# Kernel tuning notes

Hardware: AMD Instinct MI355X
Metric: run time of the kernel (lower is better)

The kernel has to match this reference:

```python
import jax, jax.numpy as jnp
import numpy as np

IN_DIM = 2
HID = 256
OUT_DIM = 1
B = 131072


def setup_inputs() -> dict:
    key = jax.random.key(0)
    ks = jax.random.split(key, 9)
    def glorot(k, shape):
        fan_in = shape[0]
        return jax.random.normal(k, shape, dtype=jnp.float32) / jnp.sqrt(jnp.float32(fan_in))
    return {
        "x": jax.random.normal(ks[0], (B, IN_DIM), dtype=jnp.float32),
        "W1": glorot(ks[1], (IN_DIM, HID)), "b1": jnp.zeros((HID,), jnp.float32),
        "W2": glorot(ks[2], (HID, HID)),    "b2": jnp.zeros((HID,), jnp.float32),
        "W3": glorot(ks[3], (HID, HID)),    "b3": jnp.zeros((HID,), jnp.float32),
        "W4": glorot(ks[4], (HID, OUT_DIM)),"b4": jnp.zeros((OUT_DIM,), jnp.float32),
    }


def reference(x, W1, b1, W2, b2, W3, b3, W4, b4):
    # Inner PINN model: tanh MLP, per-sample fn (IN_DIM,) -> (OUT_DIM,)
    def f(xi):
        h = jnp.tanh(xi @ W1 + b1)
        h = jnp.tanh(h @ W2 + b2)
        h = jnp.tanh(h @ W3 + b3)
        return h @ W4 + b4

    # Original layer computes full batch_jacobian then slices column 0.
    # Mathematically this is the directional derivative along e0, computed
    # here directly with forward-mode JVPs (same values, no wasted columns).
    e0 = jnp.zeros((IN_DIM,), x.dtype).at[0].set(1.0)

    def du_dx0(xi):  # (OUT_DIM,) : d u / d x[0]
        return jax.jvp(f, (xi,), (e0,))[1]

    def per_point(xi):
        u = f(xi)                                   # (OUT_DIM,)
        du, d2u = jax.jvp(du_dx0, (xi,), (e0,))     # du/dx0, d2u/dx0^2
        return u, du, d2u

    return jax.vmap(per_point)(x)  # each (B, OUT_DIM)
```

## Files before the change

kernel.cpp:

```cpp
#include <hip/hip_runtime.h>


#define HID 256
#define TM  32
#define LDK 264

typedef _Float16 half8 __attribute__((ext_vector_type(8)));
typedef _Float16 half4 __attribute__((ext_vector_type(4)));
typedef float    f32x4 __attribute__((ext_vector_type(4)));

__device__ __forceinline__ float fast_tanh(float z) {
    const float e = __expf(2.0f * z);
#if __has_builtin(__builtin_amdgcn_rcpf)
    const float r = __builtin_amdgcn_rcpf(e + 1.0f);
#else
    const float r = 1.0f / (e + 1.0f);
#endif
    return fmaf(-2.0f, r, 1.0f);
}

__global__ __launch_bounds__(256) void prep_w(const float* __restrict__ W2,
                                              const float* __restrict__ W3,
                                              _Float16* __restrict__ wsf) {
    const int t = blockIdx.x * 256 + threadIdx.x;
    const float* __restrict__ W = (t >> 13) ? W3 : W2;
    _Float16* hi = wsf + (size_t)(t >> 13) * 65536;
    const int r    = t & 8191;
    const int nt   = r >> 9;
    const int kc   = (r >> 6) & 7;
    const int lane = r & 63;
    const int row  = kc * 32 + ((lane >> 4) << 3);
    const int col  = nt * 16 + (lane & 15);
    half8 vh;
    #pragma unroll
    for (int j = 0; j < 8; ++j)
        vh[j] = (_Float16)W[(size_t)(row + j) * HID + col];
    *(half8*)&hi[(size_t)r * 8] = vh;
}

__global__ __launch_bounds__(512, 4) void pinn_mfma(
    const float* __restrict__ x,
    const float* __restrict__ W1, const float* __restrict__ b1,
    const float* __restrict__ b2, const float* __restrict__ b3,
    const float* __restrict__ W4, const float* __restrict__ b4,
    const _Float16* __restrict__ wsf,
    float* __restrict__ out, int B)
{
    __shared__ __align__(16) _Float16 Ahi[3][TM][LDK];
    __shared__ float psumW[8][3][TM];

    const int tid  = threadIdx.x;
    const int s0   = blockIdx.x * TM;
    const int lane = tid & 63;
    const int wave = tid >> 6;

    {
        const int m  = tid >> 4;
        const int k0 = (tid & 15) * 16;
        const float x0 = x[(s0 + m) * 2 + 0];
        const float x1 = x[(s0 + m) * 2 + 1];
        half8 vh[3][2];
        #pragma unroll
        for (int hfi = 0; hfi < 2; ++hfi) {
            #pragma unroll
            for (int j = 0; j < 8; ++j) {
                const int n = k0 + hfi * 8 + j;
                const float w0 = W1[n];
                const float w1 = W1[HID + n];
                const float z  = fmaf(x0, w0, fmaf(x1, w1, b1[n]));
                const float a  = fast_tanh(z);
                const float sN = 1.0f - a * a;
                const float ad  = sN * w0;
                const float add = -2.0f * a * ad * w0;
                vh[0][hfi][j] = (_Float16)a;
                vh[1][hfi][j] = (_Float16)ad;
                vh[2][hfi][j] = (_Float16)add;
            }
        }
        #pragma unroll
        for (int s = 0; s < 3; ++s) {
            *(half8*)&Ahi[s][m][k0]     = vh[s][0];
            *(half8*)&Ahi[s][m][k0 + 8] = vh[s][1];
        }
    }
    __syncthreads();

    const int ml = lane & 15;
    const int kq = (lane >> 4) * 8;
    const int u4 = (lane >> 4) * 4;

    #pragma unroll 1
    for (int layer = 0; layer < 2; ++layer) {
        const _Float16* __restrict__ Wh = wsf + (size_t)layer * 65536;

        f32x4 acc[3][2][2];
        #pragma unroll
        for (int s = 0; s < 3; ++s)
            #pragma unroll
            for (int nt = 0; nt < 2; ++nt)
                #pragma unroll
                for (int mt = 0; mt < 2; ++mt)
                    acc[s][nt][mt] = (f32x4){0.f, 0.f, 0.f, 0.f};

        #pragma unroll 1
        for (int kc = 0; kc < 8; ++kc) {
            half8 ah[3][2];
            #pragma unroll
            for (int s = 0; s < 3; ++s)
                #pragma unroll
                for (int mt = 0; mt < 2; ++mt)
                    ah[s][mt] = *(const half8*)&Ahi[s][mt * 16 + ml][kc * 32 + kq];
            #pragma unroll
            for (int nt = 0; nt < 2; ++nt) {
                const int strip = wave * 2 + nt;
                const size_t fi = ((size_t)((strip * 8 + kc) * 64 + lane)) * 8;
                const half8 wh = *(const half8*)&Wh[fi];
                #pragma unroll
                for (int mt = 0; mt < 2; ++mt) {
                    acc[0][nt][mt] = __builtin_amdgcn_mfma_f32_16x16x32_f16(wh, ah[0][mt], acc[0][nt][mt], 0, 0, 0);
                    acc[1][nt][mt] = __builtin_amdgcn_mfma_f32_16x16x32_f16(wh, ah[1][mt], acc[1][nt][mt], 0, 0, 0);
                    acc[2][nt][mt] = __builtin_amdgcn_mfma_f32_16x16x32_f16(wh, ah[2][mt], acc[2][nt][mt], 0, 0, 0);
                }
            }
        }

        __syncthreads();

        if (layer == 0) {
            #pragma unroll
            for (int nt = 0; nt < 2; ++nt) {
                const int ub = wave * 32 + nt * 16 + u4;
                const f32x4 bb = *(const f32x4*)&b2[ub];
                #pragma unroll
                for (int mt = 0; mt < 2; ++mt) {
                    half4 hv[3];
                    #pragma unroll
                    for (int r = 0; r < 4; ++r) {
                        const float z   = acc[0][nt][mt][r] + bb[r];
                        const float a   = fast_tanh(z);
                        const float sN  = 1.0f - a * a;
                        const float zd  = acc[1][nt][mt][r];
                        const float zdd = acc[2][nt][mt][r];
                        const float ad  = sN * zd;
                        const float add = fmaf(sN, zdd, -2.0f * a * ad * zd);
                        hv[0][r] = (_Float16)a;
                        hv[1][r] = (_Float16)ad;
                        hv[2][r] = (_Float16)add;
                    }
                    #pragma unroll
                    for (int s = 0; s < 3; ++s)
                        *(half4*)&Ahi[s][mt * 16 + ml][ub] = hv[s];
                }
            }
            __syncthreads();
        } else {
            float pd[3][2] = {{0.f, 0.f}, {0.f, 0.f}, {0.f, 0.f}};
            #pragma unroll
            for (int nt = 0; nt < 2; ++nt) {
                const int ub = wave * 32 + nt * 16 + u4;
                const f32x4 bb = *(const f32x4*)&b3[ub];
                const f32x4 w4 = *(const f32x4*)&W4[ub];
                #pragma unroll
                for (int mt = 0; mt < 2; ++mt) {
                    #pragma unroll
                    for (int r = 0; r < 4; ++r) {
                        const float z   = acc[0][nt][mt][r] + bb[r];
                        const float a   = fast_tanh(z);
                        const float sN  = 1.0f - a * a;
                        const float zd  = acc[1][nt][mt][r];
                        const float zdd = acc[2][nt][mt][r];
                        const float ad  = sN * zd;
                        const float add = fmaf(sN, zdd, -2.0f * a * ad * zd);
                        pd[0][mt] = fmaf(a,   w4[r], pd[0][mt]);
                        pd[1][mt] = fmaf(ad,  w4[r], pd[1][mt]);
                        pd[2][mt] = fmaf(add, w4[r], pd[2][mt]);
                    }
                }
            }
            #pragma unroll
            for (int s = 0; s < 3; ++s)
                #pragma unroll
                for (int mt = 0; mt < 2; ++mt) {
                    pd[s][mt] += __shfl_xor(pd[s][mt], 16, 64);
                    pd[s][mt] += __shfl_xor(pd[s][mt], 32, 64);
                }
            if (lane < 16) {
                #pragma unroll
                for (int s = 0; s < 3; ++s) {
                    psumW[wave][s][lane]      = pd[s][0];
                    psumW[wave][s][16 + lane] = pd[s][1];
                }
            }
        }
    }
    __syncthreads();

    if (tid < 96) {
        const int s = tid >> 5;
        const int m = tid & 31;
        float v = 0.f;
        #pragma unroll
        for (int w = 0; w < 8; ++w) v += psumW[w][s][m];
        if (s == 0) v += b4[0];
        out[(size_t)s * B + s0 + m] = v;
    }
}

extern "C" void kernel_launch(void* const* d_in, const int* in_sizes, int n_in,
                              void* d_out, int out_size, void* d_ws, size_t ws_size,
                              hipStream_t stream) {
    const float* x  = (const float*)d_in[0];
    const float* W1 = (const float*)d_in[1];
    const float* b1 = (const float*)d_in[2];
    const float* W2 = (const float*)d_in[3];
    const float* b2 = (const float*)d_in[4];
    const float* W3 = (const float*)d_in[5];
    const float* b3 = (const float*)d_in[6];
    const float* W4 = (const float*)d_in[7];
    const float* b4 = (const float*)d_in[8];
    float* out = (float*)d_out;

    const int B = in_sizes[0] / 2;

    prep_w<<<64, 256, 0, stream>>>(W2, W3, (_Float16*)d_ws);
    pinn_mfma<<<B / TM, 512, 0, stream>>>(x, W1, b1, b2, b3, W4, b4,
                                          (const _Float16*)d_ws, out, B);
}
```

Before: 189.3 us.

## Replace block barriers with per-wave LDS flags and switch to 32x32 MFMA tiles

Swaps the workgroup-wide __syncthreads between layers for per-wave release/acquire flags in LDS. Each wave starts on its own K-chunk and waits only on the producer wave of the chunk it needs next, with separate buffers for each layer so nothing is overwritten early. The MFMA shape moves from 16x16x32 to 32x32x16 with a matching reordered weight layout, and the weight fragments are software-prefetched one step ahead. The aim is to cut barrier stalls and let waves overlap the tanh epilogue with matrix work. The cost is doubled LDS use, dropping the min-blocks launch bound (lower occupancy), and spin-wait polling.

```diff
diff --git a/kernel.cpp b/kernel.cpp
--- a/kernel.cpp
+++ b/kernel.cpp
@@ -7,7 +7,8 @@
 
 typedef _Float16 half8 __attribute__((ext_vector_type(8)));
 typedef _Float16 half4 __attribute__((ext_vector_type(4)));
-typedef float    f32x4 __attribute__((ext_vector_type(4)));
+typedef float    f32x4  __attribute__((ext_vector_type(4)));
+typedef float    f32x16 __attribute__((ext_vector_type(16)));
 
 __device__ __forceinline__ float fast_tanh(float z) {
     const float e = __expf(2.0f * z);
@@ -19,26 +20,34 @@
     return fmaf(-2.0f, r, 1.0f);
 }
 
+__device__ __forceinline__ void wait_flag(int* f) {
+    while (__hip_atomic_load(f, __ATOMIC_ACQUIRE, __HIP_MEMORY_SCOPE_WORKGROUP) == 0)
+        __builtin_amdgcn_s_sleep(1);
+}
+__device__ __forceinline__ void set_flag(int* f) {
+    __hip_atomic_store(f, 1, __ATOMIC_RELEASE, __HIP_MEMORY_SCOPE_WORKGROUP);
+}
+
 __global__ __launch_bounds__(256) void prep_w(const float* __restrict__ W2,
                                               const float* __restrict__ W3,
                                               _Float16* __restrict__ wsf) {
     const int t = blockIdx.x * 256 + threadIdx.x;
     const float* __restrict__ W = (t >> 13) ? W3 : W2;
-    _Float16* hi = wsf + (size_t)(t >> 13) * 65536;
+    _Float16* dst = wsf + (size_t)(t >> 13) * 65536;
     const int r    = t & 8191;
-    const int nt   = r >> 9;
-    const int kc   = (r >> 6) & 7;
+    const int s    = r >> 10;
+    const int c    = (r >> 6) & 15;
     const int lane = r & 63;
-    const int row  = kc * 32 + ((lane >> 4) << 3);
-    const int col  = nt * 16 + (lane & 15);
+    const int row0 = c * 16 + ((lane >> 5) << 3);
+    const int col  = s * 32 + (lane & 31);
     half8 vh;
     #pragma unroll
     for (int j = 0; j < 8; ++j)
-        vh[j] = (_Float16)W[(size_t)(row + j) * HID + col];
-    *(half8*)&hi[(size_t)r * 8] = vh;
-}
-
-__global__ __launch_bounds__(512, 4) void pinn_mfma(
+        vh[j] = (_Float16)W[(size_t)(row0 + j) * HID + col];
+    *(half8*)&dst[(size_t)r * 8] = vh;
+}
+
+__global__ __launch_bounds__(512) void pinn_mfma(
     const float* __restrict__ x,
     const float* __restrict__ W1, const float* __restrict__ b1,
     const float* __restrict__ b2, const float* __restrict__ b3,
@@ -46,151 +55,185 @@
     const _Float16* __restrict__ wsf,
     float* __restrict__ out, int B)
 {
-    __shared__ __align__(16) _Float16 Ahi[3][TM][LDK];
-    __shared__ float psumW[8][3][TM];
+    __shared__ __align__(16) _Float16 buf1[3][TM][LDK];
+    __shared__ __align__(16) _Float16 buf2[3][TM][LDK];
+    __shared__ float psum[8][3][TM];
+    __shared__ int flag1[8];
+    __shared__ int flag2[8];
 
     const int tid  = threadIdx.x;
     const int s0   = blockIdx.x * TM;
     const int lane = tid & 63;
     const int wave = tid >> 6;
-
-    {
-        const int m  = tid >> 4;
-        const int k0 = (tid & 15) * 16;
-        const float x0 = x[(s0 + m) * 2 + 0];
-        const float x1 = x[(s0 + m) * 2 + 1];
-        half8 vh[3][2];
-        #pragma unroll
-        for (int hfi = 0; hfi < 2; ++hfi) {
+    const int n    = lane & 31;
+    const int q    = lane >> 5;
+    const int q8   = q * 8;
+
+    if (tid < 8) { flag1[tid] = 0; flag2[tid] = 0; }
+    __syncthreads();
+
+    {
+        const int u0 = wave * 32 + q * 16;
+        const float x0 = x[(s0 + n) * 2 + 0];
+        const float x1 = x[(s0 + n) * 2 + 1];
+        #pragma unroll
+        for (int g = 0; g < 4; ++g) {
+            const f32x4 wa = *(const f32x4*)&W1[u0 + g * 4];
+            const f32x4 wb = *(const f32x4*)&W1[HID + u0 + g * 4];
+            const f32x4 bv = *(const f32x4*)&b1[u0 + g * 4];
+            half4 h0, h1, h2;
             #pragma unroll
-            for (int j = 0; j < 8; ++j) {
-                const int n = k0 + hfi * 8 + j;
-                const float w0 = W1[n];
-                const float w1 = W1[HID + n];
-                const float z  = fmaf(x0, w0, fmaf(x1, w1, b1[n]));
+            for (int r = 0; r < 4; ++r) {
+                const float z  = fmaf(x0, wa[r], fmaf(x1, wb[r], bv[r]));
                 const float a  = fast_tanh(z);
                 const float sN = 1.0f - a * a;
-                const float ad  = sN * w0;
-                const float add = -2.0f * a * ad * w0;
-                vh[0][hfi][j] = (_Float16)a;
-                vh[1][hfi][j] = (_Float16)ad;
-                vh[2][hfi][j] = (_Float16)add;
-            }
-        }
-        #pragma unroll
-        for (int s = 0; s < 3; ++s) {
-            *(half8*)&Ahi[s][m][k0]     = vh[s][0];
-            *(half8*)&Ahi[s][m][k0 + 8] = vh[s][1];
-        }
-    }
-    __syncthreads();
-
-    const int ml = lane & 15;
-    const int kq = (lane >> 4) * 8;
-    const int u4 = (lane >> 4) * 4;
-
-    #pragma unroll 1
-    for (int layer = 0; layer < 2; ++layer) {
-        const _Float16* __restrict__ Wh = wsf + (size_t)layer * 65536;
-
-        f32x4 acc[3][2][2];
-        #pragma unroll
-        for (int s = 0; s < 3; ++s)
+                const float ad  = sN * wa[r];
+                const float add = -2.0f * a * ad * wa[r];
+                h0[r] = (_Float16)a;
+                h1[r] = (_Float16)ad;
+                h2[r] = (_Float16)add;
+            }
+            *(half4*)&buf1[0][n][u0 + g * 4] = h0;
+            *(half4*)&buf1[1][n][u0 + g * 4] = h1;
+            *(half4*)&buf1[2][n][u0 + g * 4] = h2;
+        }
+    }
+    if (lane == 0) set_flag(&flag1[wave]);
+
+    f32x16 acc0, acc1, acc2;
+
+    {
+        const _Float16* __restrict__ Wp = wsf;
+        #pragma unroll
+        for (int e = 0; e < 16; ++e) { acc0[e] = 0.f; acc1[e] = 0.f; acc2[e] = 0.f; }
+
+        #define WIDX(c) (((size_t)(wave * 16 + (c)) * 64 + lane) * 8)
+        half8 wA = *(const half8*)&Wp[WIDX(2 * wave)];
+        half8 wB = *(const half8*)&Wp[WIDX(2 * wave + 1)];
+        #pragma unroll
+        for (int i = 0; i < 8; ++i) {
+            const int p = (wave + i) & 7;
+            half8 wAn, wBn;
+            if (i < 7) {
+                const int pn = (wave + i + 1) & 7;
+                wAn = *(const half8*)&Wp[WIDX(2 * pn)];
+                wBn = *(const half8*)&Wp[WIDX(2 * pn + 1)];
+            }
+            if (i) wait_flag(&flag1[p]);
+            {
+                const int cc = 2 * p;
+                const half8 b0 = *(const half8*)&buf1[0][n][cc * 16 + q8];
+                const half8 b1f = *(const half8*)&buf1[1][n][cc * 16 + q8];
+                const half8 b2f = *(const half8*)&buf1[2][n][cc * 16 + q8];
+                acc0 = __builtin_amdgcn_mfma_f32_32x32x16_f16(wA, b0,  acc0, 0, 0, 0);
+                acc1 = __builtin_amdgcn_mfma_f32_32x32x16_f16(wA, b1f, acc1, 0, 0, 0);
+                acc2 = __builtin_amdgcn_mfma_f32_32x32x16_f16(wA, b2f, acc2, 0, 0, 0);
+            }
+            {
+                const int cc = 2 * p + 1;
+                const half8 b0 = *(const half8*)&buf1[0][n][cc * 16 + q8];
+                const half8 b1f = *(const half8*)&buf1[1][n][cc * 16 + q8];
+                const half8 b2f = *(const half8*)&buf1[2][n][cc * 16 + q8];
+                acc0 = __builtin_amdgcn_mfma_f32_32x32x16_f16(wB, b0,  acc0, 0, 0, 0);
+                acc1 = __builtin_amdgcn_mfma_f32_32x32x16_f16(wB, b1f, acc1, 0, 0, 0);
+                acc2 = __builtin_amdgcn_mfma_f32_32x32x16_f16(wB, b2f, acc2, 0, 0, 0);
+            }
+            wA = wAn; wB = wBn;
+        }
+    }
+
+    #pragma unroll
+    for (int g = 0; g < 4; ++g) {
+        const int ub = wave * 32 + g * 8 + q * 4;
+        const f32x4 bb = *(const f32x4*)&b2[ub];
+        half4 h0, h1, h2;
+        #pragma unroll
+        for (int r = 0; r < 4; ++r) {
+            const float z   = acc0[g * 4 + r] + bb[r];
+            const float a   = fast_tanh(z);
+            const float sN  = 1.0f - a * a;
+            const float zd  = acc1[g * 4 + r];
+            const float zdd = acc2[g * 4 + r];
+            const float ad  = sN * zd;
+            const float add = fmaf(sN, zdd, -2.0f * a * ad * zd);
+            h0[r] = (_Float16)a;
+            h1[r] = (_Float16)ad;
+            h2[r] = (_Float16)add;
+        }
+        *(half4*)&buf2[0][n][ub] = h0;
+        *(half4*)&buf2[1][n][ub] = h1;
+        *(half4*)&buf2[2][n][ub] = h2;
+    }
+    if (lane == 0) set_flag(&flag2[wave]);
+
+    {
+        const _Float16* __restrict__ Wp = wsf + 65536;
+        #pragma unroll
+        for (int e = 0; e < 16; ++e) { acc0[e] = 0.f; acc1[e] = 0.f; acc2[e] = 0.f; }
+
+        half8 wA = *(const half8*)&Wp[WIDX(2 * wave)];
+        half8 wB = *(const half8*)&Wp[WIDX(2 * wave + 1)];
+        #pragma unroll
+        for (int i = 0; i < 8; ++i) {
+            const int p = (wave + i) & 7;
+            half8 wAn, wBn;
+            if (i < 7) {
+                const int pn = (wave + i + 1) & 7;
+                wAn = *(const half8*)&Wp[WIDX(2 * pn)];
+                wBn = *(const half8*)&Wp[WIDX(2 * pn + 1)];
+            }
+            if (i) wait_flag(&flag2[p]);
+            {
+                const int cc = 2 * p;
+                const half8 b0 = *(const half8*)&buf2[0][n][cc * 16 + q8];
+                const half8 b1f = *(const half8*)&buf2[1][n][cc * 16 + q8];
+                const half8 b2f = *(const half8*)&buf2[2][n][cc * 16 + q8];
+                acc0 = __builtin_amdgcn_mfma_f32_32x32x16_f16(wA, b0,  acc0, 0, 0, 0);
+                acc1 = __builtin_amdgcn_mfma_f32_32x32x16_f16(wA, b1f, acc1, 0, 0, 0);
+                acc2 = __builtin_amdgcn_mfma_f32_32x32x16_f16(wA, b2f, acc2, 0, 0, 0);
+            }
+            {
+                const int cc = 2 * p + 1;
+                const half8 b0 = *(const half8*)&buf2[0][n][cc * 16 + q8];
+                const half8 b1f = *(const half8*)&buf2[1][n][cc * 16 + q8];
+                const half8 b2f = *(const half8*)&buf2[2][n][cc * 16 + q8];
+                acc0 = __builtin_amdgcn_mfma_f32_32x32x16_f16(wB, b0,  acc0, 0, 0, 0);
+                acc1 = __builtin_amdgcn_mfma_f32_32x32x16_f16(wB, b1f, acc1, 0, 0, 0);
+                acc2 = __builtin_amdgcn_mfma_f32_32x32x16_f16(wB, b2f, acc2, 0, 0, 0);
+            }
+            wA = wAn; wB = wBn;
+        }
+        #undef WIDX
+    }
+
+    {
+        float pd0 = 0.f, pd1 = 0.f, pd2 = 0.f;
+        #pragma unroll
+        for (int g = 0; g < 4; ++g) {
+            const int ub = wave * 32 + g * 8 + q * 4;
+            const f32x4 bb = *(const f32x4*)&b3[ub];
+            const f32x4 w4 = *(const f32x4*)&W4[ub];
             #pragma unroll
-            for (int nt = 0; nt < 2; ++nt)
-                #pragma unroll
-                for (int mt = 0; mt < 2; ++mt)
-                    acc[s][nt][mt] = (f32x4){0.f, 0.f, 0.f, 0.f};
-
-        #pragma unroll 1
-        for (int kc = 0; kc < 8; ++kc) {
-            half8 ah[3][2];
-            #pragma unroll
-            for (int s = 0; s < 3; ++s)
-                #pragma unroll
-                for (int mt = 0; mt < 2; ++mt)
-                    ah[s][mt] = *(const half8*)&Ahi[s][mt * 16 + ml][kc * 32 + kq];
-            #pragma unroll
-            for (int nt = 0; nt < 2; ++nt) {
-                const int strip = wave * 2 + nt;
-                const size_t fi = ((size_t)((strip * 8 + kc) * 64 + lane)) * 8;
-                const half8 wh = *(const half8*)&Wh[fi];
-                #pragma unroll
-                for (int mt = 0; mt < 2; ++mt) {
-                    acc[0][nt][mt] = __builtin_amdgcn_mfma_f32_16x16x32_f16(wh, ah[0][mt], acc[0][nt][mt], 0, 0, 0);
-                    acc[1][nt][mt] = __builtin_amdgcn_mfma_f32_16x16x32_f16(wh, ah[1][mt], acc[1][nt][mt], 0, 0, 0);
-                    acc[2][nt][mt] = __builtin_amdgcn_mfma_f32_16x16x32_f16(wh, ah[2][mt], acc[2][nt][mt], 0, 0, 0);
-                }
-            }
-        }
-
-        __syncthreads();
-
-        if (layer == 0) {
-            #pragma unroll
-            for (int nt = 0; nt < 2; ++nt) {
-                const int ub = wave * 32 + nt * 16 + u4;
-                const f32x4 bb = *(const f32x4*)&b2[ub];
-                #pragma unroll
-                for (int mt = 0; mt < 2; ++mt) {
-                    half4 hv[3];
-                    #pragma unroll
-                    for (int r = 0; r < 4; ++r) {
-                        const float z   = acc[0][nt][mt][r] + bb[r];
-                        const float a   = fast_tanh(z);
-                        const float sN  = 1.0f - a * a;
-                        const float zd  = acc[1][nt][mt][r];
-                        const float zdd = acc[2][nt][mt][r];
-                        const float ad  = sN * zd;
-                        const float add = fmaf(sN, zdd, -2.0f * a * ad * zd);
-                        hv[0][r] = (_Float16)a;
-                        hv[1][r] = (_Float16)ad;
-                        hv[2][r] = (_Float16)add;
-                    }
-                    #pragma unroll
-                    for (int s = 0; s < 3; ++s)
-                        *(half4*)&Ahi[s][mt * 16 + ml][ub] = hv[s];
-                }
-            }
-            __syncthreads();
-        } else {
-            float pd[3][2] = {{0.f, 0.f}, {0.f, 0.f}, {0.f, 0.f}};
-            #pragma unroll
-            for (int nt = 0; nt < 2; ++nt) {
-                const int ub = wave * 32 + nt * 16 + u4;
-                const f32x4 bb = *(const f32x4*)&b3[ub];
-                const f32x4 w4 = *(const f32x4*)&W4[ub];
-                #pragma unroll
-                for (int mt = 0; mt < 2; ++mt) {
-                    #pragma unroll
-                    for (int r = 0; r < 4; ++r) {
-                        const float z   = acc[0][nt][mt][r] + bb[r];
-                        const float a   = fast_tanh(z);
-                        const float sN  = 1.0f - a * a;
-                        const float zd  = acc[1][nt][mt][r];
-                        const float zdd = acc[2][nt][mt][r];
-                        const float ad  = sN * zd;
-                        const float add = fmaf(sN, zdd, -2.0f * a * ad * zd);
-                        pd[0][mt] = fmaf(a,   w4[r], pd[0][mt]);
-                        pd[1][mt] = fmaf(ad,  w4[r], pd[1][mt]);
-                        pd[2][mt] = fmaf(add, w4[r], pd[2][mt]);
-                    }
-                }
-            }
-            #pragma unroll
-            for (int s = 0; s < 3; ++s)
-                #pragma unroll
-                for (int mt = 0; mt < 2; ++mt) {
-                    pd[s][mt] += __shfl_xor(pd[s][mt], 16, 64);
-                    pd[s][mt] += __shfl_xor(pd[s][mt], 32, 64);
-                }
-            if (lane < 16) {
-                #pragma unroll
-                for (int s = 0; s < 3; ++s) {
-                    psumW[wave][s][lane]      = pd[s][0];
-                    psumW[wave][s][16 + lane] = pd[s][1];
-                }
-            }
+            for (int r = 0; r < 4; ++r) {
+                const float z   = acc0[g * 4 + r] + bb[r];
+                const float a   = fast_tanh(z);
+                const float sN  = 1.0f - a * a;
+                const float zd  = acc1[g * 4 + r];
+                const float zdd = acc2[g * 4 + r];
+                const float ad  = sN * zd;
+                const float add = fmaf(sN, zdd, -2.0f * a * ad * zd);
+                pd0 = fmaf(a,   w4[r], pd0);
+                pd1 = fmaf(ad,  w4[r], pd1);
+                pd2 = fmaf(add, w4[r], pd2);
+            }
+        }
+        pd0 += __shfl_xor(pd0, 32, 64);
+        pd1 += __shfl_xor(pd1, 32, 64);
+        pd2 += __shfl_xor(pd2, 32, 64);
+        if (lane < 32) {
+            psum[wave][0][lane] = pd0;
+            psum[wave][1][lane] = pd1;
+            psum[wave][2][lane] = pd2;
         }
     }
     __syncthreads();
@@ -200,7 +243,7 @@
         const int m = tid & 31;
         float v = 0.f;
         #pragma unroll
-        for (int w = 0; w < 8; ++w) v += psumW[w][s][m];
+        for (int w = 0; w < 8; ++w) v += psum[w][s][m];
         if (s == 0) v += b4[0];
         out[(size_t)s * B + s0 + m] = v;
     }
```

New measurement: 200.0 us. 1.06x slower.

## Split tile into two 16-row halves and overlap tanh epilogues with MFMA

Applied to the files above, without the earlier changes.

Splits each 32-sample tile into two 16-row halves with separate LDS buffers. The tanh/derivative epilogue of one half is interleaved with the MFMA loop of the other, including the first-layer input activations. Each wave now holds its W2/W3 fragments in registers for the whole layer and packs fp16 pairs with cvt_pkrtz. This aims to hide the transcendental and conversion work behind matrix ops, at the cost of many more live VGPRs and the loss of the explicit occupancy hint in the launch bounds.

```diff
diff --git a/kernel.cpp b/kernel.cpp
--- a/kernel.cpp
+++ b/kernel.cpp
@@ -2,12 +2,11 @@
 
 
 #define HID 256
-#define TM  32
 #define LDK 264
 
-typedef _Float16 half8 __attribute__((ext_vector_type(8)));
-typedef _Float16 half4 __attribute__((ext_vector_type(4)));
-typedef float    f32x4 __attribute__((ext_vector_type(4)));
+typedef _Float16 half8  __attribute__((ext_vector_type(8)));
+typedef __fp16   fp16x2 __attribute__((ext_vector_type(2)));
+typedef float    f32x4  __attribute__((ext_vector_type(4)));
 
 __device__ __forceinline__ float fast_tanh(float z) {
     const float e = __expf(2.0f * z);
@@ -19,12 +18,20 @@
     return fmaf(-2.0f, r, 1.0f);
 }
 
+__device__ __forceinline__ unsigned pkh(float lo, float hi) {
+    union { fp16x2 h; unsigned u; } c;
+    c.h = __builtin_amdgcn_cvt_pkrtz(lo, hi);
+    return c.u;
+}
+
+#define MFMA16(a, b, c) __builtin_amdgcn_mfma_f32_16x16x32_f16((a), (b), (c), 0, 0, 0)
+
 __global__ __launch_bounds__(256) void prep_w(const float* __restrict__ W2,
                                               const float* __restrict__ W3,
                                               _Float16* __restrict__ wsf) {
     const int t = blockIdx.x * 256 + threadIdx.x;
     const float* __restrict__ W = (t >> 13) ? W3 : W2;
-    _Float16* hi = wsf + (size_t)(t >> 13) * 65536;
+    _Float16* dst = wsf + (size_t)(t >> 13) * 65536;
     const int r    = t & 8191;
     const int nt   = r >> 9;
     const int kc   = (r >> 6) & 7;
@@ -35,10 +42,10 @@
     #pragma unroll
     for (int j = 0; j < 8; ++j)
         vh[j] = (_Float16)W[(size_t)(row + j) * HID + col];
-    *(half8*)&hi[(size_t)r * 8] = vh;
-}
-
-__global__ __launch_bounds__(512, 4) void pinn_mfma(
+    *(half8*)&dst[(size_t)r * 8] = vh;
+}
+
+__global__ __launch_bounds__(512) void pinn_mfma(
     const float* __restrict__ x,
     const float* __restrict__ W1, const float* __restrict__ b1,
     const float* __restrict__ b2, const float* __restrict__ b3,
@@ -46,164 +53,283 @@
     const _Float16* __restrict__ wsf,
     float* __restrict__ out, int B)
 {
-    __shared__ __align__(16) _Float16 Ahi[3][TM][LDK];
-    __shared__ float psumW[8][3][TM];
+    __shared__ __align__(16) _Float16 bufA[3][16][LDK];
+    __shared__ __align__(16) _Float16 bufB[3][16][LDK];
+    float* const psumA = (float*)&bufA[0][0][0];
+    float* const psumB = (float*)&bufB[0][0][0];
 
     const int tid  = threadIdx.x;
-    const int s0   = blockIdx.x * TM;
     const int lane = tid & 63;
     const int wave = tid >> 6;
-
-    {
-        const int m  = tid >> 4;
-        const int k0 = (tid & 15) * 16;
-        const float x0 = x[(s0 + m) * 2 + 0];
-        const float x1 = x[(s0 + m) * 2 + 1];
-        half8 vh[3][2];
-        #pragma unroll
-        for (int hfi = 0; hfi < 2; ++hfi) {
-            #pragma unroll
-            for (int j = 0; j < 8; ++j) {
-                const int n = k0 + hfi * 8 + j;
-                const float w0 = W1[n];
-                const float w1 = W1[HID + n];
-                const float z  = fmaf(x0, w0, fmaf(x1, w1, b1[n]));
-                const float a  = fast_tanh(z);
-                const float sN = 1.0f - a * a;
-                const float ad  = sN * w0;
-                const float add = -2.0f * a * ad * w0;
-                vh[0][hfi][j] = (_Float16)a;
-                vh[1][hfi][j] = (_Float16)ad;
-                vh[2][hfi][j] = (_Float16)add;
-            }
-        }
-        #pragma unroll
-        for (int s = 0; s < 3; ++s) {
-            *(half8*)&Ahi[s][m][k0]     = vh[s][0];
-            *(half8*)&Ahi[s][m][k0 + 8] = vh[s][1];
-        }
-    }
-    __syncthreads();
-
-    const int ml = lane & 15;
-    const int kq = (lane >> 4) * 8;
-    const int u4 = (lane >> 4) * 4;
-
-    #pragma unroll 1
-    for (int layer = 0; layer < 2; ++layer) {
-        const _Float16* __restrict__ Wh = wsf + (size_t)layer * 65536;
-
-        f32x4 acc[3][2][2];
-        #pragma unroll
-        for (int s = 0; s < 3; ++s)
-            #pragma unroll
-            for (int nt = 0; nt < 2; ++nt)
-                #pragma unroll
-                for (int mt = 0; mt < 2; ++mt)
-                    acc[s][nt][mt] = (f32x4){0.f, 0.f, 0.f, 0.f};
-
-        #pragma unroll 1
-        for (int kc = 0; kc < 8; ++kc) {
-            half8 ah[3][2];
-            #pragma unroll
-            for (int s = 0; s < 3; ++s)
-                #pragma unroll
-                for (int mt = 0; mt < 2; ++mt)
-                    ah[s][mt] = *(const half8*)&Ahi[s][mt * 16 + ml][kc * 32 + kq];
-            #pragma unroll
-            for (int nt = 0; nt < 2; ++nt) {
-                const int strip = wave * 2 + nt;
-                const size_t fi = ((size_t)((strip * 8 + kc) * 64 + lane)) * 8;
-                const half8 wh = *(const half8*)&Wh[fi];
-                #pragma unroll
-                for (int mt = 0; mt < 2; ++mt) {
-                    acc[0][nt][mt] = __builtin_amdgcn_mfma_f32_16x16x32_f16(wh, ah[0][mt], acc[0][nt][mt], 0, 0, 0);
-                    acc[1][nt][mt] = __builtin_amdgcn_mfma_f32_16x16x32_f16(wh, ah[1][mt], acc[1][nt][mt], 0, 0, 0);
-                    acc[2][nt][mt] = __builtin_amdgcn_mfma_f32_16x16x32_f16(wh, ah[2][mt], acc[2][nt][mt], 0, 0, 0);
-                }
-            }
-        }
-
-        __syncthreads();
-
-        if (layer == 0) {
-            #pragma unroll
-            for (int nt = 0; nt < 2; ++nt) {
-                const int ub = wave * 32 + nt * 16 + u4;
-                const f32x4 bb = *(const f32x4*)&b2[ub];
-                #pragma unroll
-                for (int mt = 0; mt < 2; ++mt) {
-                    half4 hv[3];
-                    #pragma unroll
-                    for (int r = 0; r < 4; ++r) {
-                        const float z   = acc[0][nt][mt][r] + bb[r];
-                        const float a   = fast_tanh(z);
-                        const float sN  = 1.0f - a * a;
-                        const float zd  = acc[1][nt][mt][r];
-                        const float zdd = acc[2][nt][mt][r];
-                        const float ad  = sN * zd;
-                        const float add = fmaf(sN, zdd, -2.0f * a * ad * zd);
-                        hv[0][r] = (_Float16)a;
-                        hv[1][r] = (_Float16)ad;
-                        hv[2][r] = (_Float16)add;
-                    }
-                    #pragma unroll
-                    for (int s = 0; s < 3; ++s)
-                        *(half4*)&Ahi[s][mt * 16 + ml][ub] = hv[s];
-                }
-            }
-            __syncthreads();
-        } else {
-            float pd[3][2] = {{0.f, 0.f}, {0.f, 0.f}, {0.f, 0.f}};
-            #pragma unroll
-            for (int nt = 0; nt < 2; ++nt) {
-                const int ub = wave * 32 + nt * 16 + u4;
-                const f32x4 bb = *(const f32x4*)&b3[ub];
-                const f32x4 w4 = *(const f32x4*)&W4[ub];
-                #pragma unroll
-                for (int mt = 0; mt < 2; ++mt) {
-                    #pragma unroll
-                    for (int r = 0; r < 4; ++r) {
-                        const float z   = acc[0][nt][mt][r] + bb[r];
-                        const float a   = fast_tanh(z);
-                        const float sN  = 1.0f - a * a;
-                        const float zd  = acc[1][nt][mt][r];
-                        const float zdd = acc[2][nt][mt][r];
-                        const float ad  = sN * zd;
-                        const float add = fmaf(sN, zdd, -2.0f * a * ad * zd);
-                        pd[0][mt] = fmaf(a,   w4[r], pd[0][mt]);
-                        pd[1][mt] = fmaf(ad,  w4[r], pd[1][mt]);
-                        pd[2][mt] = fmaf(add, w4[r], pd[2][mt]);
-                    }
-                }
-            }
-            #pragma unroll
-            for (int s = 0; s < 3; ++s)
-                #pragma unroll
-                for (int mt = 0; mt < 2; ++mt) {
-                    pd[s][mt] += __shfl_xor(pd[s][mt], 16, 64);
-                    pd[s][mt] += __shfl_xor(pd[s][mt], 32, 64);
-                }
-            if (lane < 16) {
-                #pragma unroll
-                for (int s = 0; s < 3; ++s) {
-                    psumW[wave][s][lane]      = pd[s][0];
-                    psumW[wave][s][16 + lane] = pd[s][1];
-                }
-            }
+    const int n    = lane & 15;
+    const int q    = lane >> 4;
+    const int q8   = q * 8;
+    const int sA   = blockIdx.x * 32;
+    const int u0   = wave * 32 + q * 8;
+
+    #define WIDX(t_, c_) ((size_t)(((wave * 2 + (t_)) * 8 + (c_)) * 64 + lane) * 8)
+
+    f32x4 accA[3][2], accB[3][2];
+    half8 wc[2][8];
+
+    {
+        const float2 xv  = *(const float2*)&x[(size_t)(sA + n) * 2];
+        const f32x4 wa0 = *(const f32x4*)&W1[u0];
+        const f32x4 wa1 = *(const f32x4*)&W1[u0 + 4];
+        const f32x4 wb0 = *(const f32x4*)&W1[HID + u0];
+        const f32x4 wb1 = *(const f32x4*)&W1[HID + u0 + 4];
+        const f32x4 bb0 = *(const f32x4*)&b1[u0];
+        const f32x4 bb1 = *(const f32x4*)&b1[u0 + 4];
+        unsigned pk[3][4];
+        float pa = 0.f, pdv = 0.f, p2 = 0.f;
+        #pragma unroll
+        for (int j = 0; j < 8; ++j) {
+            const float w0 = (j < 4) ? wa0[j & 3] : wa1[j & 3];
+            const float w1v = (j < 4) ? wb0[j & 3] : wb1[j & 3];
+            const float bb = (j < 4) ? bb0[j & 3] : bb1[j & 3];
+            const float z  = fmaf(xv.x, w0, fmaf(xv.y, w1v, bb));
+            const float a  = fast_tanh(z);
+            const float sN = fmaf(-a, a, 1.0f);
+            const float ad = sN * w0;
+            const float add = -2.0f * a * ad * w0;
+            if (j & 1) {
+                pk[0][j >> 1] = pkh(pa, a);
+                pk[1][j >> 1] = pkh(pdv, ad);
+                pk[2][j >> 1] = pkh(p2, add);
+            } else { pa = a; pdv = ad; p2 = add; }
+        }
+        #pragma unroll
+        for (int s = 0; s < 3; ++s) {
+            uint4 v; v.x = pk[s][0]; v.y = pk[s][1]; v.z = pk[s][2]; v.w = pk[s][3];
+            *(uint4*)&bufA[s][n][u0] = v;
+        }
+    }
+    __syncthreads();
+
+    {
+        #pragma unroll
+        for (int c = 0; c < 8; ++c) {
+            wc[0][c] = *(const half8*)&wsf[WIDX(0, c)];
+            wc[1][c] = *(const half8*)&wsf[WIDX(1, c)];
+        }
+        #pragma unroll
+        for (int s = 0; s < 3; ++s) {
+            accA[s][0] = (f32x4){0.f, 0.f, 0.f, 0.f};
+            accA[s][1] = (f32x4){0.f, 0.f, 0.f, 0.f};
+        }
+        const float2 xv  = *(const float2*)&x[(size_t)(sA + 16 + n) * 2];
+        const f32x4 wa0 = *(const f32x4*)&W1[u0];
+        const f32x4 wa1 = *(const f32x4*)&W1[u0 + 4];
+        const f32x4 wb0 = *(const f32x4*)&W1[HID + u0];
+        const f32x4 wb1 = *(const f32x4*)&W1[HID + u0 + 4];
+        const f32x4 bb0 = *(const f32x4*)&b1[u0];
+        const f32x4 bb1 = *(const f32x4*)&b1[u0 + 4];
+        unsigned pk[3][4];
+        float pa = 0.f, pdv = 0.f, p2 = 0.f;
+        #pragma unroll
+        for (int c = 0; c < 8; ++c) {
+            const half8 f0 = *(const half8*)&bufA[0][n][c * 32 + q8];
+            const half8 f1 = *(const half8*)&bufA[1][n][c * 32 + q8];
+            const half8 f2 = *(const half8*)&bufA[2][n][c * 32 + q8];
+            accA[0][0] = MFMA16(wc[0][c], f0, accA[0][0]);
+            accA[1][0] = MFMA16(wc[0][c], f1, accA[1][0]);
+            accA[2][0] = MFMA16(wc[0][c], f2, accA[2][0]);
+            accA[0][1] = MFMA16(wc[1][c], f0, accA[0][1]);
+            accA[1][1] = MFMA16(wc[1][c], f1, accA[1][1]);
+            accA[2][1] = MFMA16(wc[1][c], f2, accA[2][1]);
+            const float w0 = (c < 4) ? wa0[c & 3] : wa1[c & 3];
+            const float w1v = (c < 4) ? wb0[c & 3] : wb1[c & 3];
+            const float bb = (c < 4) ? bb0[c & 3] : bb1[c & 3];
+            const float z  = fmaf(xv.x, w0, fmaf(xv.y, w1v, bb));
+            const float a  = fast_tanh(z);
+            const float sN = fmaf(-a, a, 1.0f);
+            const float ad = sN * w0;
+            const float add = -2.0f * a * ad * w0;
+            if (c & 1) {
+                pk[0][c >> 1] = pkh(pa, a);
+                pk[1][c >> 1] = pkh(pdv, ad);
+                pk[2][c >> 1] = pkh(p2, add);
+            } else { pa = a; pdv = ad; p2 = add; }
+        }
+        #pragma unroll
+        for (int s = 0; s < 3; ++s) {
+            uint4 v; v.x = pk[s][0]; v.y = pk[s][1]; v.z = pk[s][2]; v.w = pk[s][3];
+            *(uint4*)&bufB[s][n][u0] = v;
+        }
+    }
+    __syncthreads();
+
+    const f32x4 bb2a = *(const f32x4*)&b2[(wave * 2 + 0) * 16 + q * 4];
+    const f32x4 bb2b = *(const f32x4*)&b2[(wave * 2 + 1) * 16 + q * 4];
+
+    {
+        #pragma unroll
+        for (int s = 0; s < 3; ++s) {
+            accB[s][0] = (f32x4){0.f, 0.f, 0.f, 0.f};
+            accB[s][1] = (f32x4){0.f, 0.f, 0.f, 0.f};
+        }
+        float pa = 0.f, pdv = 0.f, p2 = 0.f;
+        #pragma unroll
+        for (int c = 0; c < 8; ++c) {
+            const half8 f0 = *(const half8*)&bufB[0][n][c * 32 + q8];
+            const half8 f1 = *(const half8*)&bufB[1][n][c * 32 + q8];
+            const half8 f2 = *(const half8*)&bufB[2][n][c * 32 + q8];
+            accB[0][0] = MFMA16(wc[0][c], f0, accB[0][0]);
+            accB[1][0] = MFMA16(wc[0][c], f1, accB[1][0]);
+            accB[2][0] = MFMA16(wc[0][c], f2, accB[2][0]);
+            accB[0][1] = MFMA16(wc[1][c], f0, accB[0][1]);
+            accB[1][1] = MFMA16(wc[1][c], f1, accB[1][1]);
+            accB[2][1] = MFMA16(wc[1][c], f2, accB[2][1]);
+            const int t = c >> 2, r = c & 3;
+            const float z   = accA[0][t][r] + ((c < 4) ? bb2a[r] : bb2b[r]);
+            const float a   = fast_tanh(z);
+            const float sN  = fmaf(-a, a, 1.0f);
+            const float zd  = accA[1][t][r];
+            const float zdd = accA[2][t][r];
+            const float ad  = sN * zd;
+            const float tt  = a * ad * zd;
+            const float add = fmaf(sN, zdd, -2.0f * tt);
+            if (r & 1) {
+                const int ub = (wave * 2 + t) * 16 + q * 4 + (r - 1);
+                *(unsigned*)&bufA[0][n][ub] = pkh(pa, a);
+                *(unsigned*)&bufA[1][n][ub] = pkh(pdv, ad);
+                *(unsigned*)&bufA[2][n][ub] = pkh(p2, add);
+            } else { pa = a; pdv = ad; p2 = add; }
+        }
+    }
+    __syncthreads();
+
+    {
+        #pragma unroll
+        for (int c = 0; c < 8; ++c) {
+            wc[0][c] = *(const half8*)&wsf[65536 + WIDX(0, c)];
+            wc[1][c] = *(const half8*)&wsf[65536 + WIDX(1, c)];
+        }
+        #pragma unroll
+        for (int s = 0; s < 3; ++s) {
+            accA[s][0] = (f32x4){0.f, 0.f, 0.f, 0.f};
+            accA[s][1] = (f32x4){0.f, 0.f, 0.f, 0.f};
+        }
+        float pa = 0.f, pdv = 0.f, p2 = 0.f;
+        #pragma unroll
+        for (int c = 0; c < 8; ++c) {
+            const half8 f0 = *(const half8*)&bufA[0][n][c * 32 + q8];
+            const half8 f1 = *(const half8*)&bufA[1][n][c * 32 + q8];
+            const half8 f2 = *(const half8*)&bufA[2][n][c * 32 + q8];
+            accA[0][0] = MFMA16(wc[0][c], f0, accA[0][0]);
+            accA[1][0] = MFMA16(wc[0][c], f1, accA[1][0]);
+            accA[2][0] = MFMA16(wc[0][c], f2, accA[2][0]);
+            accA[0][1] = MFMA16(wc[1][c], f0, accA[0][1]);
+            accA[1][1] = MFMA16(wc[1][c], f1, accA[1][1]);
+            accA[2][1] = MFMA16(wc[1][c], f2, accA[2][1]);
+            const int t = c >> 2, r = c & 3;
+            const float z   = accB[0][t][r] + ((c < 4) ? bb2a[r] : bb2b[r]);
+            const float a   = fast_tanh(z);
+            const float sN  = fmaf(-a, a, 1.0f);
+            const float zd  = accB[1][t][r];
+            const float zdd = accB[2][t][r];
+            const float ad  = sN * zd;
+            const float tt  = a * ad * zd;
+            const float add = fmaf(sN, zdd, -2.0f * tt);
+            if (r & 1) {
+                const int ub = (wave * 2 + t) * 16 + q * 4 + (r - 1);
+                *(unsigned*)&bufB[0][n][ub] = pkh(pa, a);
+                *(unsigned*)&bufB[1][n][ub] = pkh(pdv, ad);
+                *(unsigned*)&bufB[2][n][ub] = pkh(p2, add);
+            } else { pa = a; pdv = ad; p2 = add; }
+        }
+    }
+    __syncthreads();
+
+    const f32x4 bb3a = *(const f32x4*)&b3[(wave * 2 + 0) * 16 + q * 4];
+    const f32x4 bb3b = *(const f32x4*)&b3[(wave * 2 + 1) * 16 + q * 4];
+    const f32x4 w4a  = *(const f32x4*)&W4[(wave * 2 + 0) * 16 + q * 4];
+    const f32x4 w4b  = *(const f32x4*)&W4[(wave * 2 + 1) * 16 + q * 4];
+
+    {
+        #pragma unroll
+        for (int s = 0; s < 3; ++s) {
+            accB[s][0] = (f32x4){0.f, 0.f, 0.f, 0.f};
+            accB[s][1] = (f32x4){0.f, 0.f, 0.f, 0.f};
+        }
+        float pd0 = 0.f, pd1 = 0.f, pd2 = 0.f;
+        #pragma unroll
+        for (int c = 0; c < 8; ++c) {
+            const half8 f0 = *(const half8*)&bufB[0][n][c * 32 + q8];
+            const half8 f1 = *(const half8*)&bufB[1][n][c * 32 + q8];
+            const half8 f2 = *(const half8*)&bufB[2][n][c * 32 + q8];
+            accB[0][0] = MFMA16(wc[0][c], f0, accB[0][0]);
+            accB[1][0] = MFMA16(wc[0][c], f1, accB[1][0]);
+            accB[2][0] = MFMA16(wc[0][c], f2, accB[2][0]);
+            accB[0][1] = MFMA16(wc[1][c], f0, accB[0][1]);
+            accB[1][1] = MFMA16(wc[1][c], f1, accB[1][1]);
+            accB[2][1] = MFMA16(wc[1][c], f2, accB[2][1]);
+            const int t = c >> 2, r = c & 3;
+            const float z   = accA[0][t][r] + ((c < 4) ? bb3a[r] : bb3b[r]);
+            const float a   = fast_tanh(z);
+            const float sN  = fmaf(-a, a, 1.0f);
+            const float zd  = accA[1][t][r];
+            const float zdd = accA[2][t][r];
+            const float ad  = sN * zd;
+            const float tt  = a * ad * zd;
+            const float add = fmaf(sN, zdd, -2.0f * tt);
+            const float w4v = (c < 4) ? w4a[r] : w4b[r];
+            pd0 = fmaf(a,   w4v, pd0);
+            pd1 = fmaf(ad,  w4v, pd1);
+            pd2 = fmaf(add, w4v, pd2);
+        }
+        pd0 += __shfl_xor(pd0, 16, 64); pd0 += __shfl_xor(pd0, 32, 64);
+        pd1 += __shfl_xor(pd1, 16, 64); pd1 += __shfl_xor(pd1, 32, 64);
+        pd2 += __shfl_xor(pd2, 16, 64); pd2 += __shfl_xor(pd2, 32, 64);
+        if (lane < 16) {
+            psumA[(wave * 3 + 0) * 16 + lane] = pd0;
+            psumA[(wave * 3 + 1) * 16 + lane] = pd1;
+            psumA[(wave * 3 + 2) * 16 + lane] = pd2;
+        }
+    }
+    __syncthreads();
+
+    {
+        float pd0 = 0.f, pd1 = 0.f, pd2 = 0.f;
+        #pragma unroll
+        for (int c = 0; c < 8; ++c) {
+            const int t = c >> 2, r = c & 3;
+            const float z   = accB[0][t][r] + ((c < 4) ? bb3a[r] : bb3b[r]);
+            const float a   = fast_tanh(z);
+            const float sN  = fmaf(-a, a, 1.0f);
+            const float zd  = accB[1][t][r];
+            const float zdd = accB[2][t][r];
+            const float ad  = sN * zd;
+            const float tt  = a * ad * zd;
+            const float add = fmaf(sN, zdd, -2.0f * tt);
+            const float w4v = (c < 4) ? w4a[r] : w4b[r];
+            pd0 = fmaf(a,   w4v, pd0);
+            pd1 = fmaf(ad,  w4v, pd1);
+            pd2 = fmaf(add, w4v, pd2);
+        }
+        pd0 += __shfl_xor(pd0, 16, 64); pd0 += __shfl_xor(pd0, 32, 64);
+        pd1 += __shfl_xor(pd1, 16, 64); pd1 += __shfl_xor(pd1, 32, 64);
+        pd2 += __shfl_xor(pd2, 16, 64); pd2 += __shfl_xor(pd2, 32, 64);
+        if (lane < 16) {
+            psumB[(wave * 3 + 0) * 16 + lane] = pd0;
+            psumB[(wave * 3 + 1) * 16 + lane] = pd1;
+            psumB[(wave * 3 + 2) * 16 + lane] = pd2;
         }
     }
     __syncthreads();
 
     if (tid < 96) {
-        const int s = tid >> 5;
-        const int m = tid & 31;
+        const int s  = tid >> 5;
+        const int m  = tid & 31;
+        const float* ps = (m & 16) ? psumB : psumA;
+        const int nn = m & 15;
         float v = 0.f;
         #pragma unroll
-        for (int w = 0; w < 8; ++w) v += psumW[w][s][m];
+        for (int w = 0; w < 8; ++w) v += ps[(w * 3 + s) * 16 + nn];
         if (s == 0) v += b4[0];
-        out[(size_t)s * B + s0 + m] = v;
-    }
+        out[(size_t)s * B + sA + m] = v;
+    }
+    #undef WIDX
 }
 
 extern "C" void kernel_launch(void* const* d_in, const int* in_sizes, int n_in,
@@ -223,6 +349,6 @@
     const int B = in_sizes[0] / 2;
 
     prep_w<<<64, 256, 0, stream>>>(W2, W3, (_Float16*)d_ws);
-    pinn_mfma<<<B / TM, 512, 0, stream>>>(x, W1, b1, b2, b3, W4, b4,
+    pinn_mfma<<<B / 32, 512, 0, stream>>>(x, W1, b1, b2, b3, W4, b4,
                                           (const _Float16*)d_ws, out, B);
 }
```

After: 199.3 us. +5.3%, slower.
